# Kernel optimization log

Measured on AMD Instinct MI355X. Metric: run time of the kernel, lower is better.

Reference implementation:

```python
import jax, jax.numpy as jnp
import numpy as np

B, Nq, Nk, R = 4, 1024, 1024, 256
NH, DK, DV = 8, 64, 64


def setup_inputs() -> dict:
    key = jax.random.key(0)
    ks = jax.random.split(key, 16)
    mk = lambda k, shape, s=1.0: jax.random.normal(k, shape, dtype=jnp.float32) * s
    inp = {
        'Q_real': mk(ks[0], (B, Nq, R)), 'Q_imag': mk(ks[1], (B, Nq, R)),
        'K_real': mk(ks[2], (B, Nk, R)), 'K_imag': mk(ks[3], (B, Nk, R)),
        'V_real': mk(ks[4], (B, Nk, R)), 'V_imag': mk(ks[5], (B, Nk, R)),
        'WQ_r': mk(ks[6], (NH * DK, R), 0.02), 'WQ_i': mk(ks[7], (NH * DK, R), 0.02),
        'WK_r': mk(ks[8], (NH * DK, R), 0.02), 'WK_i': mk(ks[9], (NH * DK, R), 0.02),
        'WV_r': mk(ks[10], (NH * DV, R), 0.02), 'WV_i': mk(ks[11], (NH * DV, R), 0.02),
        'WO_r': mk(ks[12], (R, NH * DV), 0.02), 'WO_i': mk(ks[13], (R, NH * DV), 0.02),
        'mask': jax.random.randint(ks[14], (B, Nk), 0, 2).astype(bool),
    }
    return inp


def _complex_linear(x, w_r, w_i):
    # x: complex [..., in]; weights real [out, in]. Same math as 4 real matmuls.
    w = (w_r + 1j * w_i).astype(jnp.complex64)
    return x @ w.T


def reference(Q_real, Q_imag, K_real, K_imag, V_real, V_imag,
              WQ_r, WQ_i, WK_r, WK_i, WV_r, WV_i, WO_r, WO_i, mask):
    Q = (Q_real + 1j * Q_imag).astype(jnp.complex64)
    K = (K_real + 1j * K_imag).astype(jnp.complex64)
    V = (V_real + 1j * V_imag).astype(jnp.complex64)

    Qp = _complex_linear(Q, WQ_r, WQ_i).reshape(B, Nq, NH, DK).transpose(0, 2, 1, 3)
    Kp = _complex_linear(K, WK_r, WK_i).reshape(B, Nk, NH, DK).transpose(0, 2, 1, 3)
    Vp = _complex_linear(V, WV_r, WV_i).reshape(B, Nk, NH, DV).transpose(0, 2, 1, 3)

    # complex scores [B, NH, Nq, Nk]; conj on K matches torch .conj().transpose
    scores = jnp.einsum('bhqd,bhkd->bhqk', Qp, jnp.conj(Kp)) / jnp.sqrt(jnp.float32(DK))
    scores_abs = jnp.abs(scores)

    m = mask[:, None, None, :]                    # [B,1,1,Nk]
    valid = jnp.any(mask, axis=-1)[:, None, None, None]  # [B,1,1,1] valid query rows
    masked = jnp.where(m, scores_abs, -jnp.inf)
    # avoid all -inf rows feeding softmax (those rows are zeroed afterwards)
    safe = jnp.where(valid, masked, 0.0)
    w = jax.nn.softmax(safe, axis=-1)
    w = jnp.where(valid, w, 0.0)

    attn = jnp.einsum('bhqk,bhkd->bhqd', w.astype(Vp.dtype), Vp)
    attn = attn.transpose(0, 2, 1, 3).reshape(B, Nq, NH * DV)
    return _complex_linear(attn, WO_r, WO_i)
```

## Files before the change

### kernel.cpp

```cpp
#include <hip/hip_runtime.h>
#include <math.h>

#define NBATCH 4
#define NSEQ   1024
#define RD     256
#define NHEAD  8
#define HD     64
#define NHD    512

typedef __attribute__((ext_vector_type(8))) short  short8;
typedef __attribute__((ext_vector_type(4))) short  short4v;
typedef __attribute__((ext_vector_type(4))) float  float4v;

#define MFMA16(a,b,c) __builtin_amdgcn_mfma_f32_16x16x32_bf16(a,b,c,0,0,0)

typedef const void __attribute__((address_space(1)))* gas_t;
typedef void __attribute__((address_space(3)))* las_t;
#define GLOAD16(g, l) __builtin_amdgcn_global_load_lds((gas_t)(g), (las_t)(l), 16, 0, 0)

static __device__ __forceinline__ unsigned short f2b(float f) {
    union { float f; unsigned u; } x; x.f = f;
    unsigned r = x.u + 0x7fffu + ((x.u >> 16) & 1u);
    return (unsigned short)(r >> 16);
}
static __device__ __forceinline__ void st4(short* dst, float4v v) {
    short4v p;
    p[0] = (short)f2b(v[0]); p[1] = (short)f2b(v[1]);
    p[2] = (short)f2b(v[2]); p[3] = (short)f2b(v[3]);
    *(short4v*)dst = p;
}

struct ConvArgs { const float* src[15]; short* dst[15]; int n4[15]; };

__global__ __launch_bounds__(256) void convert_bf16(ConvArgs ca)
{
    const int a = blockIdx.y;
    if (a == 14) {
        if (blockIdx.x != 0) return;
        __shared__ int isByteLayout;
        const int t = threadIdx.x;
        if (t == 0) isByteLayout = 0;
        __syncthreads();
        const int* mi = (const int*)ca.src[14];
        #pragma unroll
        for (int j = 0; j < 4; j++) {
            int v = mi[t*4 + j];
            if (v & ~1) isByteLayout = 1;
        }
        __syncthreads();
        unsigned char* nm = (unsigned char*)ca.dst[14];
        const unsigned char* mb = (const unsigned char*)ca.src[14];
        if (isByteLayout) {
            #pragma unroll
            for (int j = 0; j < 16; j++) { int k = t*16 + j; nm[k] = mb[k] ? 1 : 0; }
        } else {
            #pragma unroll
            for (int j = 0; j < 16; j++) { int k = t*16 + j; nm[k] = mi[k] ? 1 : 0; }
        }
        return;
    }
    const float* __restrict__ s = ca.src[a];
    short* __restrict__ d = ca.dst[a];
    const int n4 = ca.n4[a];
    for (int i = blockIdx.x*256 + threadIdx.x; i < n4; i += gridDim.x*256) {
        float4v v = *(const float4v*)(s + (size_t)i*4);
        st4(d + (size_t)i*4, v);
    }
}

struct ProjArgs {
    const short* Xr[3]; const short* Xi[3];
    const short* Wr[3]; const short* Wi[3];
    short* Yr[3]; short* Yi[3];
};

__global__ __launch_bounds__(256) void cgemm_proj(ProjArgs pa)
{
    __shared__ short sX[2][128][64];
    __shared__ short sW[2][64][64];
    const int z = blockIdx.z;
    const short* __restrict__ X_r = pa.Xr[z];
    const short* __restrict__ X_i = pa.Xi[z];
    const short* __restrict__ W_r = pa.Wr[z];
    const short* __restrict__ W_i = pa.Wi[z];
    short* __restrict__ Y_r = pa.Yr[z];
    short* __restrict__ Y_i = pa.Yi[z];
    const int transposeOut = (z == 2);

    const int tid  = threadIdx.x;
    const int lane = tid & 63, wave = tid >> 6;
    const int quad = lane >> 4, l16 = lane & 15;
    const int sw8  = l16 & 7;
    const int rsub = lane >> 3;
    const int colg = (lane & 7) ^ rsub;
    const int n0 = blockIdx.x * 64, m0 = blockIdx.y * 128;

    const short nk = (short)0x8000;
    const short8 neg = {nk,nk,nk,nk,nk,nk,nk,nk};

    float4v zf = {0.f,0.f,0.f,0.f};
    float4v Yr[2][4], Yi[2][4];
    #pragma unroll
    for (int ms = 0; ms < 2; ms++)
        #pragma unroll
        for (int t = 0; t < 4; t++) { Yr[ms][t] = zf; Yi[ms][t] = zf; }

    for (int kc = 0; kc < RD; kc += 64) {
        __syncthreads();
        if (wave < 2) {
            const short* gp = wave ? X_i : X_r;
            short* lp = wave ? &sX[1][0][0] : &sX[0][0][0];
            #pragma unroll
            for (int j = 0; j < 16; j++) {
                int row = j*8 + rsub;
                GLOAD16(gp + (size_t)(m0 + row)*RD + kc + colg*8, lp + j*512);
            }
        } else {
            const short* gp = (wave == 3) ? W_i : W_r;
            short* lp = (wave == 3) ? &sW[1][0][0] : &sW[0][0][0];
            #pragma unroll
            for (int j = 0; j < 8; j++) {
                int row = j*8 + rsub;
                GLOAD16(gp + (size_t)(n0 + row)*RD + kc + colg*8, lp + j*512);
            }
        }
        __syncthreads();
        short8 fxr[2][2], fxi[2][2], fxin[2][2];
        #pragma unroll
        for (int ms = 0; ms < 2; ms++)
            #pragma unroll
            for (int ds = 0; ds < 2; ds++) {
                int row = wave*32 + ms*16 + l16;
                int u = ((ds*4 + quad) ^ sw8) * 8;
                fxr[ms][ds]  = *(short8*)&sX[0][row][u];
                fxi[ms][ds]  = *(short8*)&sX[1][row][u];
                fxin[ms][ds] = fxi[ms][ds] ^ neg;
            }
        #pragma unroll
        for (int t = 0; t < 4; t++)
            #pragma unroll
            for (int ds = 0; ds < 2; ds++) {
                int u = ((ds*4 + quad) ^ sw8) * 8;
                short8 wr = *(short8*)&sW[0][t*16 + l16][u];
                short8 wi = *(short8*)&sW[1][t*16 + l16][u];
                #pragma unroll
                for (int ms = 0; ms < 2; ms++) {
                    Yr[ms][t] = MFMA16(fxr[ms][ds],  wr, Yr[ms][t]);
                    Yr[ms][t] = MFMA16(fxin[ms][ds], wi, Yr[ms][t]);
                    Yi[ms][t] = MFMA16(fxr[ms][ds],  wi, Yi[ms][t]);
                    Yi[ms][t] = MFMA16(fxi[ms][ds],  wr, Yi[ms][t]);
                }
            }
    }

    const int b = m0 >> 10, h = n0 >> 6, nb = m0 & 1023;
    short* sT = &sX[0][0][0];
    short* Yp[2] = { Y_r, Y_i };
    #pragma unroll
    for (int p = 0; p < 2; p++) {
        __syncthreads();
        #pragma unroll
        for (int ms = 0; ms < 2; ms++)
            #pragma unroll
            for (int t = 0; t < 4; t++)
                #pragma unroll
                for (int r = 0; r < 4; r++) {
                    float v = p ? Yi[ms][t][r] : Yr[ms][t][r];
                    int rr = wave*32 + ms*16 + quad*4 + r;
                    int cc = t*16 + l16;
                    if (!transposeOut) sT[rr*68 + cc]  = (short)f2b(v);
                    else               sT[cc*132 + rr] = (short)f2b(v);
                }
        __syncthreads();
        #pragma unroll
        for (int it = 0; it < 4; it++) {
            int idx = it*256 + tid;
            int rr, c8;
            size_t o;
            const short* sp;
            if (!transposeOut) {
                rr = idx >> 3; c8 = (idx & 7)*8;
                sp = &sT[rr*68 + c8];
                o = (((size_t)(b*NHEAD + h))*NSEQ + nb + rr)*HD + c8;
            } else {
                rr = idx >> 4; c8 = (idx & 15)*8;
                sp = &sT[rr*132 + c8];
                o = (((size_t)(b*NHEAD + h))*HD + rr)*NSEQ + nb + c8;
            }
            short4v a = *(short4v*)sp;
            short4v bq = *(short4v*)(sp + 4);
            short8 v8 = { a[0],a[1],a[2],a[3], bq[0],bq[1],bq[2],bq[3] };
            *(short8*)&Yp[p][o] = v8;
        }
    }
}

__global__ __launch_bounds__(512) void attn_mfma(
    const short* __restrict__ Qp_r, const short* __restrict__ Qp_i,
    const short* __restrict__ Kp_r, const short* __restrict__ Kp_i,
    const short* __restrict__ Vp_r, const short* __restrict__ Vp_i,
    const unsigned char* __restrict__ mask,
    short* __restrict__ Ar, short* __restrict__ Ai)
{
    __shared__ __align__(16) char smem[44032];
    short (*sK)[64][64] = (short(*)[64][64])smem;
    short (*sV)[64][64] = (short(*)[64][64])(smem + 16384);
    short (*sP)[16][40] = (short(*)[16][40])(smem + 32768);
    unsigned char* smask = (unsigned char*)(smem + 43008);

    const int tid  = threadIdx.x;
    const int lane = tid & 63, wave = tid >> 6;
    const int quad = lane >> 4, l16 = lane & 15;
    const int sw8  = l16 & 7;
    const int qstrip = wave >> 1;
    const int khalf  = wave & 1;
    const int qt = blockIdx.x >> 5;
    const int bh = blockIdx.x & 31;
    const int b  = bh >> 3, h = bh & 7;
    const size_t base = (size_t)bh * (NSEQ*HD);

    const int rsub = lane >> 3;
    const int colg = (lane & 7) ^ rsub;

    if (tid < 256) ((int*)smask)[tid] = ((const int*)(mask + b*NSEQ))[tid];

    {
        const int q0 = qt*64;
        const short* gp = (wave >> 2) ? Qp_i : Qp_r;
        short* lp = (wave >> 2) ? &sK[1][0][0] : &sK[0][0][0];
        #pragma unroll
        for (int jj = 0; jj < 2; jj++) {
            int j = (wave & 3)*2 + jj;
            int row = j*8 + rsub;
            GLOAD16(gp + base + (size_t)(q0 + row)*HD + colg*8, lp + j*512);
        }
    }
    __syncthreads();

    short8 fqr[2], fqi[2], fqrn[2];
    {
        const short nk = (short)0x8000;
        short8 neg = {nk,nk,nk,nk,nk,nk,nk,nk};
        const int qrow = qstrip*16 + l16;
        #pragma unroll
        for (int ds = 0; ds < 2; ds++) {
            int u = ((ds*4 + quad) ^ sw8) * 8;
            fqr[ds]  = *(short8*)&sK[0][qrow][u];
            fqi[ds]  = *(short8*)&sK[1][qrow][u];
            fqrn[ds] = fqr[ds] ^ neg;
        }
    }

    float4v zf = {0.f,0.f,0.f,0.f};
    float4v Or[4], Oi[4];
    float lrow[4];
    #pragma unroll
    for (int t = 0; t < 4; t++) { Or[t] = zf; Oi[t] = zf; }
    #pragma unroll
    for (int r = 0; r < 4; r++) lrow[r] = 0.f;

    const float C2 = 0.18033688f;

    for (int kt = 0; kt < 16; kt++) {
        const int k0 = kt*64;
        __syncthreads();
        {
            const int plane = wave >> 1;
            const short* gp; short* lp; int isV;
            if      (plane == 0) { gp = Kp_r; lp = &sK[0][0][0]; isV = 0; }
            else if (plane == 1) { gp = Kp_i; lp = &sK[1][0][0]; isV = 0; }
            else if (plane == 2) { gp = Vp_r; lp = &sV[0][0][0]; isV = 1; }
            else                 { gp = Vp_i; lp = &sV[1][0][0]; isV = 1; }
            #pragma unroll
            for (int jj = 0; jj < 4; jj++) {
                int j = (wave & 1)*4 + jj;
                int row = j*8 + rsub;
                const short* g = isV
                    ? gp + base + (size_t)row*NSEQ + k0 + colg*8
                    : gp + base + (size_t)(k0 + row)*HD + colg*8;
                GLOAD16(g, lp + j*512);
            }
        }
        __syncthreads();

        float4v Sr[2], Si[2];
        Sr[0] = zf; Sr[1] = zf; Si[0] = zf; Si[1] = zf;
        #pragma unroll
        for (int t = 0; t < 2; t++)
            #pragma unroll
            for (int ds = 0; ds < 2; ds++) {
                int u = ((ds*4 + quad) ^ sw8) * 8;
                int krow = khalf*32 + t*16 + l16;
                short8 kr = *(short8*)&sK[0][krow][u];
                short8 ki = *(short8*)&sK[1][krow][u];
                Sr[t] = MFMA16(fqr[ds],  kr, Sr[t]);
                Sr[t] = MFMA16(fqi[ds],  ki, Sr[t]);
                Si[t] = MFMA16(fqi[ds],  kr, Si[t]);
                Si[t] = MFMA16(fqrn[ds], ki, Si[t]);
            }

        #pragma unroll
        for (int t = 0; t < 2; t++) {
            bool mv = smask[k0 + khalf*32 + t*16 + l16] != 0;
            #pragma unroll
            for (int r = 0; r < 4; r++) {
                float a = Sr[t][r], c = Si[t][r];
                float x = fmaf(a, a, c*c);
                float s = __builtin_amdgcn_sqrtf(x);
                float e = mv ? __builtin_amdgcn_exp2f(C2 * s) : 0.f;
                lrow[r] += e;
                sP[wave][quad*4 + r][t*16 + l16] = (short)f2b(e);
            }
        }

        {
            short8 fp = *(short8*)&sP[wave][l16][quad*8];
            #pragma unroll
            for (int t = 0; t < 4; t++) {
                int u = ((khalf*4 + quad) ^ sw8) * 8;
                short8 vr = *(short8*)&sV[0][t*16 + l16][u];
                short8 vi = *(short8*)&sV[1][t*16 + l16][u];
                Or[t] = MFMA16(fp, vr, Or[t]);
                Oi[t] = MFMA16(fp, vi, Oi[t]);
            }
        }
    }

    __syncthreads();
    float* sC = (float*)smem;
    float* sL = (float*)(smem + 32768);
    if (khalf == 1) {
        #pragma unroll
        for (int t = 0; t < 4; t++)
            #pragma unroll
            for (int r = 0; r < 4; r++) {
                int o8 = ((qstrip*4 + t)*64 + lane)*8 + r*2;
                sC[o8]     = Or[t][r];
                sC[o8 + 1] = Oi[t][r];
            }
        int lo = (qstrip*64 + lane)*4;
        #pragma unroll
        for (int r = 0; r < 4; r++) sL[lo + r] = lrow[r];
    }
    __syncthreads();
    if (khalf == 0) {
        #pragma unroll
        for (int t = 0; t < 4; t++)
            #pragma unroll
            for (int r = 0; r < 4; r++) {
                int o8 = ((qstrip*4 + t)*64 + lane)*8 + r*2;
                Or[t][r] += sC[o8];
                Oi[t][r] += sC[o8 + 1];
            }
        int lo = (qstrip*64 + lane)*4;
        float inv[4];
        #pragma unroll
        for (int r = 0; r < 4; r++) {
            float ls = lrow[r] + sL[lo + r];
            ls += __shfl_xor(ls, 1, 64);
            ls += __shfl_xor(ls, 2, 64);
            ls += __shfl_xor(ls, 4, 64);
            ls += __shfl_xor(ls, 8, 64);
            inv[r] = (ls > 0.f) ? 1.f/ls : 0.f;
        }
        #pragma unroll
        for (int t = 0; t < 4; t++)
            #pragma unroll
            for (int r = 0; r < 4; r++) {
                int q = qt*64 + qstrip*16 + quad*4 + r;
                int d = t*16 + l16;
                size_t o = ((size_t)(b*NSEQ + q))*NHD + h*HD + d;
                Ar[o] = (short)f2b(Or[t][r] * inv[r]);
                Ai[o] = (short)f2b(Oi[t][r] * inv[r]);
            }
    }
}

__global__ __launch_bounds__(256) void cgemm_out(
    const short* __restrict__ A_r, const short* __restrict__ A_i,
    const short* __restrict__ W_r, const short* __restrict__ W_i,
    float* __restrict__ Out, int writeImagPlane)
{
    __shared__ short sA[2][64][64];
    __shared__ short sW[2][32][64];
    const int tid  = threadIdx.x;
    const int lane = tid & 63, wave = tid >> 6;
    const int quad = lane >> 4, l16 = lane & 15;
    const int sw8  = l16 & 7;
    const int rsub = lane >> 3;
    const int colg = (lane & 7) ^ rsub;
    const int n0 = blockIdx.x * 32, m0 = blockIdx.y * 64;

    const short nk = (short)0x8000;
    const short8 neg = {nk,nk,nk,nk,nk,nk,nk,nk};

    float4v zf = {0.f,0.f,0.f,0.f};
    float4v Yr[2], Yi[2];
    #pragma unroll
    for (int t = 0; t < 2; t++) { Yr[t] = zf; Yi[t] = zf; }

    for (int kc = 0; kc < NHD; kc += 64) {
        __syncthreads();
        {
            if (wave < 2) {
                const short* gp = wave ? A_i : A_r;
                short* lp = wave ? &sA[1][0][0] : &sA[0][0][0];
                #pragma unroll
                for (int j = 0; j < 8; j++) {
                    int row = j*8 + rsub;
                    GLOAD16(gp + (size_t)(m0 + row)*NHD + kc + colg*8, lp + j*512);
                }
            } else {
                const short* gp = (wave == 3) ? W_i : W_r;
                short* lp = (wave == 3) ? &sW[1][0][0] : &sW[0][0][0];
                #pragma unroll
                for (int j = 0; j < 4; j++) {
                    int row = j*8 + rsub;
                    GLOAD16(gp + (size_t)(n0 + row)*NHD + kc + colg*8, lp + j*512);
                }
            }
        }
        __syncthreads();
        short8 far[2], fai[2], fain[2];
        #pragma unroll
        for (int ds = 0; ds < 2; ds++) {
            int u = ((ds*4 + quad) ^ sw8) * 8;
            far[ds]  = *(short8*)&sA[0][wave*16 + l16][u];
            fai[ds]  = *(short8*)&sA[1][wave*16 + l16][u];
            fain[ds] = fai[ds] ^ neg;
        }
        #pragma unroll
        for (int t = 0; t < 2; t++)
            #pragma unroll
            for (int ds = 0; ds < 2; ds++) {
                int u = ((ds*4 + quad) ^ sw8) * 8;
                short8 wr = *(short8*)&sW[0][t*16 + l16][u];
                short8 wi = *(short8*)&sW[1][t*16 + l16][u];
                Yr[t] = MFMA16(far[ds],  wr, Yr[t]);
                Yr[t] = MFMA16(fain[ds], wi, Yr[t]);
                Yi[t] = MFMA16(far[ds],  wi, Yi[t]);
                Yi[t] = MFMA16(fai[ds],  wr, Yi[t]);
            }
    }
    const size_t TOT = (size_t)NBATCH * NSEQ * RD;
    #pragma unroll
    for (int t = 0; t < 2; t++)
        #pragma unroll
        for (int r = 0; r < 4; r++) {
            int row = m0 + wave*16 + quad*4 + r;
            int col = n0 + t*16 + l16;
            size_t o = (size_t)row*RD + col;
            Out[o] = Yr[t][r];
            if (writeImagPlane) Out[o + TOT] = Yi[t][r];
        }
}

extern "C" void kernel_launch(void* const* d_in, const int* in_sizes, int n_in,
                              void* d_out, int out_size, void* d_ws, size_t ws_size,
                              hipStream_t stream)
{
    float* out = (float*)d_out;

    const size_t P = (size_t)NBATCH * NHEAD * NSEQ * HD;
    const size_t H = (size_t)NBATCH * NSEQ * RD;
    const size_t WSZ = (size_t)NHD * RD;

    short* bws = (short*)d_ws;
    short* Qpr = bws + 0*P;  short* Qpi = bws + 1*P;
    short* Kpr = bws + 2*P;  short* Kpi = bws + 3*P;
    short* Vpr = bws + 4*P;  short* Vpi = bws + 5*P;
    short* conv = bws + 6*P;
    short* cX[6]; for (int i = 0; i < 6; i++) cX[i] = conv + i*H;
    short* cW[6]; for (int i = 0; i < 6; i++) cW[i] = conv + 6*H + i*WSZ;
    short* cWOr = conv + 6*H + 6*WSZ;
    short* cWOi = conv + 6*H + 7*WSZ;
    short* Apr = conv;
    short* Api = conv + P;
    unsigned char* nmask = (unsigned char*)(conv + 6*H + 8*WSZ);

    const size_t TOT = (size_t)NBATCH * NSEQ * RD;
    const int writeImagPlane = ((size_t)out_size >= 2*TOT) ? 1 : 0;

    ConvArgs ca;
    for (int i = 0; i < 6; i++) {
        ca.src[i] = (const float*)d_in[i];  ca.dst[i] = cX[i];  ca.n4[i] = (int)(H/4);
    }
    for (int i = 0; i < 6; i++) {
        ca.src[6+i] = (const float*)d_in[6+i]; ca.dst[6+i] = cW[i]; ca.n4[6+i] = (int)(WSZ/4);
    }
    ca.src[12] = (const float*)d_in[12]; ca.dst[12] = cWOr; ca.n4[12] = (int)(WSZ/4);
    ca.src[13] = (const float*)d_in[13]; ca.dst[13] = cWOi; ca.n4[13] = (int)(WSZ/4);
    ca.src[14] = (const float*)d_in[14]; ca.dst[14] = (short*)nmask; ca.n4[14] = 0;

    ProjArgs pa;
    pa.Xr[0] = cX[0]; pa.Xi[0] = cX[1];
    pa.Xr[1] = cX[2]; pa.Xi[1] = cX[3];
    pa.Xr[2] = cX[4]; pa.Xi[2] = cX[5];
    pa.Wr[0] = cW[0]; pa.Wi[0] = cW[1];
    pa.Wr[1] = cW[2]; pa.Wi[1] = cW[3];
    pa.Wr[2] = cW[4]; pa.Wi[2] = cW[5];
    pa.Yr[0] = Qpr; pa.Yi[0] = Qpi;
    pa.Yr[1] = Kpr; pa.Yi[1] = Kpi;
    pa.Yr[2] = Vpr; pa.Yi[2] = Vpi;

    convert_bf16<<<dim3(256, 15), 256, 0, stream>>>(ca);
    cgemm_proj<<<dim3(8, 32, 3), 256, 0, stream>>>(pa);
    attn_mfma<<<dim3(512), 512, 0, stream>>>(Qpr, Qpi, Kpr, Kpi, Vpr, Vpi,
                                             nmask, Apr, Api);
    cgemm_out<<<dim3(8, 64), 256, 0, stream>>>(Apr, Api, cWOr, cWOi, out,
                                               writeImagPlane);
}
```

Measured before the change: 174.1 us.

## Double-buffer K/V tiles in attention kernel and load Q fragments from global

The K/V LDS staging in the attention kernel becomes a two-buffer ping-pong. The global-to-LDS load for tile kt+1 is issued right after the barrier, so it overlaps the MFMA and softmax work on tile kt, and one barrier per iteration is removed. Q fragments are now read straight from global memory into registers, which drops the initial LDS staging pass and its barrier. In exchange, shared memory grows from about 44 KB to about 77 KB per block, which may cut the number of resident blocks per CU.

Result: no change. 173.1 us (median of 2 runs) (-0.6%).

```diff
diff --git a/kernel.cpp b/kernel.cpp
--- a/kernel.cpp
+++ b/kernel.cpp
@@ -202,11 +202,9 @@
     const unsigned char* __restrict__ mask,
     short* __restrict__ Ar, short* __restrict__ Ai)
 {
-    __shared__ __align__(16) char smem[44032];
-    short (*sK)[64][64] = (short(*)[64][64])smem;
-    short (*sV)[64][64] = (short(*)[64][64])(smem + 16384);
-    short (*sP)[16][40] = (short(*)[16][40])(smem + 32768);
-    unsigned char* smask = (unsigned char*)(smem + 43008);
+    __shared__ __align__(16) char smem[76800];
+    short (*sP)[16][40] = (short(*)[16][40])(smem + 65536);
+    unsigned char* smask = (unsigned char*)(smem + 75776);
 
     const int tid  = threadIdx.x;
     const int lane = tid & 63, wave = tid >> 6;
@@ -224,31 +222,21 @@
 
     if (tid < 256) ((int*)smask)[tid] = ((const int*)(mask + b*NSEQ))[tid];
 
-    {
-        const int q0 = qt*64;
-        const short* gp = (wave >> 2) ? Qp_i : Qp_r;
-        short* lp = (wave >> 2) ? &sK[1][0][0] : &sK[0][0][0];
-        #pragma unroll
-        for (int jj = 0; jj < 2; jj++) {
-            int j = (wave & 3)*2 + jj;
-            int row = j*8 + rsub;
-            GLOAD16(gp + base + (size_t)(q0 + row)*HD + colg*8, lp + j*512);
-        }
-    }
-    __syncthreads();
-
+    const int splane = wave >> 1;
+    const short* sgp = (splane == 0) ? Kp_r : (splane == 1) ? Kp_i
+                     : (splane == 2) ? Vp_r : Vp_i;
+    const int sisV = (splane >= 2);
+    const int soff = splane * 8192;
+
+    const short nk = (short)0x8000;
+    const short8 neg = {nk,nk,nk,nk,nk,nk,nk,nk};
     short8 fqr[2], fqi[2], fqrn[2];
-    {
-        const short nk = (short)0x8000;
-        short8 neg = {nk,nk,nk,nk,nk,nk,nk,nk};
-        const int qrow = qstrip*16 + l16;
-        #pragma unroll
-        for (int ds = 0; ds < 2; ds++) {
-            int u = ((ds*4 + quad) ^ sw8) * 8;
-            fqr[ds]  = *(short8*)&sK[0][qrow][u];
-            fqi[ds]  = *(short8*)&sK[1][qrow][u];
-            fqrn[ds] = fqr[ds] ^ neg;
-        }
+    #pragma unroll
+    for (int ds = 0; ds < 2; ds++) {
+        size_t qo = base + (size_t)(qt*64 + qstrip*16 + l16)*HD + ds*32 + quad*8;
+        fqr[ds]  = *(const short8*)&Qp_r[qo];
+        fqi[ds]  = *(const short8*)&Qp_i[qo];
+        fqrn[ds] = fqr[ds] ^ neg;
     }
 
     float4v zf = {0.f,0.f,0.f,0.f};
@@ -261,27 +249,42 @@
 
     const float C2 = 0.18033688f;
 
+    {
+        short* lp = (short*)(smem + soff);
+        #pragma unroll
+        for (int jj = 0; jj < 4; jj++) {
+            int j = (wave & 1)*4 + jj;
+            int row = j*8 + rsub;
+            const short* g = sisV
+                ? sgp + base + (size_t)row*NSEQ + colg*8
+                : sgp + base + (size_t)row*HD + colg*8;
+            GLOAD16(g, lp + j*512);
+        }
+    }
+
     for (int kt = 0; kt < 16; kt++) {
-        const int k0 = kt*64;
-        __syncthreads();
-        {
-            const int plane = wave >> 1;
-            const short* gp; short* lp; int isV;
-            if      (plane == 0) { gp = Kp_r; lp = &sK[0][0][0]; isV = 0; }
-            else if (plane == 1) { gp = Kp_i; lp = &sK[1][0][0]; isV = 0; }
-            else if (plane == 2) { gp = Vp_r; lp = &sV[0][0][0]; isV = 1; }
-            else                 { gp = Vp_i; lp = &sV[1][0][0]; isV = 1; }
+        __syncthreads();
+
+        if (kt + 1 < 16) {
+            const int kn = (kt + 1) * 64;
+            short* lp = (short*)(smem + ((kt + 1) & 1)*32768 + soff);
             #pragma unroll
             for (int jj = 0; jj < 4; jj++) {
                 int j = (wave & 1)*4 + jj;
                 int row = j*8 + rsub;
-                const short* g = isV
-                    ? gp + base + (size_t)row*NSEQ + k0 + colg*8
-                    : gp + base + (size_t)(k0 + row)*HD + colg*8;
+                const short* g = sisV
+                    ? sgp + base + (size_t)row*NSEQ + kn + colg*8
+                    : sgp + base + (size_t)(kn + row)*HD + colg*8;
                 GLOAD16(g, lp + j*512);
             }
         }
-        __syncthreads();
+
+        const char* buf = smem + (kt & 1)*32768;
+        short (*sK0)[64] = (short(*)[64])(buf);
+        short (*sK1)[64] = (short(*)[64])(buf + 8192);
+        short (*sV0)[64] = (short(*)[64])(buf + 16384);
+        short (*sV1)[64] = (short(*)[64])(buf + 24576);
+        const int k0 = kt*64;
 
         float4v Sr[2], Si[2];
         Sr[0] = zf; Sr[1] = zf; Si[0] = zf; Si[1] = zf;
@@ -291,8 +294,8 @@
             for (int ds = 0; ds < 2; ds++) {
                 int u = ((ds*4 + quad) ^ sw8) * 8;
                 int krow = khalf*32 + t*16 + l16;
-                short8 kr = *(short8*)&sK[0][krow][u];
-                short8 ki = *(short8*)&sK[1][krow][u];
+                short8 kr = *(short8*)&sK0[krow][u];
+                short8 ki = *(short8*)&sK1[krow][u];
                 Sr[t] = MFMA16(fqr[ds],  kr, Sr[t]);
                 Sr[t] = MFMA16(fqi[ds],  ki, Sr[t]);
                 Si[t] = MFMA16(fqi[ds],  kr, Si[t]);
@@ -318,8 +321,8 @@
             #pragma unroll
             for (int t = 0; t < 4; t++) {
                 int u = ((khalf*4 + quad) ^ sw8) * 8;
-                short8 vr = *(short8*)&sV[0][t*16 + l16][u];
-                short8 vi = *(short8*)&sV[1][t*16 + l16][u];
+                short8 vr = *(short8*)&sV0[t*16 + l16][u];
+                short8 vi = *(short8*)&sV1[t*16 + l16][u];
                 Or[t] = MFMA16(fp, vr, Or[t]);
                 Oi[t] = MFMA16(fp, vi, Oi[t]);
             }
```
